# Kernel tuning notes

Measured on AMD Instinct MI355X. Metric: run time of the kernel, lower is better.

## Reference

```python
import jax, jax.numpy as jnp
import numpy as np

NH = 8          # n_heads
EPS = 1e-12     # layer_norm_eps


def _ln(x, g, b, eps=EPS):
    m = x.mean(-1, keepdims=True)
    v = jnp.var(x, axis=-1, keepdims=True)
    return (x - m) / jnp.sqrt(v + eps) * g + b


def _heads(x):
    # [B,S,H] -> [B,NH,S,H/NH]
    B, S, H = x.shape
    return x.reshape(B, S, NH, H // NH).transpose(0, 2, 1, 3)


def setup_inputs() -> dict:
    B, S, H, INNER = 32, 512, 512, 2048
    n_items = 50000
    std = 0.02
    ks = list(jax.random.split(jax.random.key(0), 20))
    inp = {}
    inp['x'] = jax.random.normal(ks[0], (B, S, H), jnp.float32)
    inp['value_input'] = jax.random.normal(ks[1], (B, S, H), jnp.float32)
    inp['beha_emb'] = jax.random.normal(ks[2], (B, S, H), jnp.float32)
    inp['pos_table'] = std * jax.random.normal(ks[3], (S, H), jnp.float32)
    names = ['q', 'k', 'v', 'pk', 'pq', 'bk', 'bq', 'd']
    for i, n in enumerate(names):
        inp['W' + n] = std * jax.random.normal(ks[4 + i], (H, H), jnp.float32)
        inp['b' + n] = jnp.zeros((H,), jnp.float32)
    inp['ln_g'] = jnp.ones((H,), jnp.float32)
    inp['ln_b'] = jnp.zeros((H,), jnp.float32)
    inp['W1'] = std * jax.random.normal(ks[12], (H, INNER), jnp.float32)
    inp['b1'] = jnp.zeros((INNER,), jnp.float32)
    inp['W2'] = std * jax.random.normal(ks[13], (INNER, H), jnp.float32)
    inp['b2'] = jnp.zeros((H,), jnp.float32)
    inp['ln2_g'] = jnp.ones((H,), jnp.float32)
    inp['ln2_b'] = jnp.zeros((H,), jnp.float32)
    inp['item_seq'] = jax.random.randint(ks[14], (B, S), 0, n_items, jnp.int32)
    return inp


def reference(x, value_input, beha_emb, pos_table, Wq, bq, Wk, bk, Wv, bv,
              Wpk, bpk, Wpq, bpq, Wbk, bbk, Wbq, bbq, Wd, bd, ln_g, ln_b,
              W1, b1, W2, b2, ln2_g, ln2_b, item_seq):
    B, S, H = x.shape
    dh = H // NH
    pos = pos_table[:S][None]  # [1,S,H] position_embedding(arange(S))

    q = _heads(x @ Wq + bq)
    k = _heads(x @ Wk + bk)
    v = _heads(value_input @ Wv + bv + value_input)  # value(value_input) + value_input
    pk = _heads(jnp.broadcast_to(pos @ Wpk + bpk, (B, S, H)))
    pq = _heads(jnp.broadcast_to(pos @ Wpq + bpq, (B, S, H)))
    bhk = _heads(beha_emb @ Wbk + bbk)
    bhq = _heads(beha_emb @ Wbq + bbq)

    # disentangled score: q.k^T + q.((beha_k+pos_k)/2)^T + ((beha_q+pos_q)/2).k^T
    scores = (jnp.einsum('bhqd,bhkd->bhqk', q, k)
              + jnp.einsum('bhqd,bhkd->bhqk', q, (bhk + pk) * 0.5)
              + jnp.einsum('bhqd,bhkd->bhqk', (bhq + pq) * 0.5, k))
    scores = scores / (dh ** 0.5)

    # causal + padding mask: (1 - mask) * -10000
    valid = item_seq > 0                              # [B,S]
    causal = jnp.tril(jnp.ones((S, S), bool))         # [S,S]
    ok = valid[:, None, None, :] & causal[None, None]
    scores = scores + jnp.where(ok, 0.0, -10000.0)

    probs = jax.nn.softmax(scores, axis=-1)
    ctx = jnp.einsum('bhqk,bhkd->bhqd', probs, v)
    ctx = ctx.transpose(0, 2, 1, 3).reshape(B, S, H)

    attn_out = _ln(ctx @ Wd + bd + x, ln_g, ln_b)

    # FeedForward (RecBole): dense1 -> gelu -> dense2 -> LN(residual)
    h = jax.nn.gelu(attn_out @ W1 + b1, approximate=False)
    h = h @ W2 + b2
    return _ln(h + attn_out, ln2_g, ln2_b)
```

## Files before the change

kernel.cpp:

```cpp
#include <hip/hip_runtime.h>
#include <math.h>


typedef unsigned short u16;
typedef __attribute__((ext_vector_type(8))) short bf16x8;
typedef __attribute__((ext_vector_type(4))) float f32x4;

#define NM 16384

__device__ __forceinline__ u16 f2b(float f) {
  union { float f; unsigned u; } x; x.f = f;
  return (u16)((x.u + 0x7fffu + ((x.u >> 16) & 1u)) >> 16);
}
__device__ __forceinline__ float b2f(u16 u) {
  union { unsigned u; float f; } x; x.u = ((unsigned)u) << 16; return x.f;
}
__device__ __forceinline__ f32x4 mfma16(bf16x8 a, bf16x8 b, f32x4 c) {
  return __builtin_amdgcn_mfma_f32_16x16x32_bf16(a, b, c, 0, 0, 0);
}
__device__ __forceinline__ void gl16(const u16* g, u16* l) {
  __builtin_amdgcn_global_load_lds(
      (const __attribute__((address_space(1))) unsigned int*)(const void*)g,
      (__attribute__((address_space(3))) unsigned int*)(void*)l, 16, 0, 0);
}

__device__ __forceinline__ void gemm_kloop(
    const u16* pa, const u16* pb, size_t lda, size_t ldb, int kiters,
    const u16* As, const u16* Bs, u16* sa, u16* sb, f32x4 (&acc)[4][4])
{
  const int tid = threadIdx.x;
  const int wave = tid>>6, lane = tid&63, quad = lane>>4, l16 = lane&15;
  const int wm = wave>>1, wn = wave&1;
  const int sw = l16 & 7;
  for (int it = 0; it < kiters; ++it) {
    const u16* pak = pa + it*64;
    const u16* pbk = pb + it*64;
    gl16(pak,          sa);
    gl16(pak + 32*lda, sa + 2048);
    gl16(pak + 64*lda, sa + 4096);
    gl16(pak + 96*lda, sa + 6144);
    gl16(pbk,          sb);
    gl16(pbk + 32*ldb, sb + 2048);
    gl16(pbk + 64*ldb, sb + 4096);
    gl16(pbk + 96*ldb, sb + 6144);
    __syncthreads();
    #pragma unroll
    for (int ks = 0; ks < 2; ++ks) {
      bf16x8 af[4], bf[4];
      #pragma unroll
      for (int i = 0; i < 4; ++i)
        af[i] = *(const bf16x8*)&As[(wm*64 + i*16 + l16)*64 + (((ks*4+quad)^sw)*8)];
      #pragma unroll
      for (int j = 0; j < 4; ++j)
        bf[j] = *(const bf16x8*)&Bs[(wn*64 + j*16 + l16)*64 + (((ks*4+quad)^sw)*8)];
      #pragma unroll
      for (int i = 0; i < 4; ++i)
        #pragma unroll
        for (int j = 0; j < 4; ++j)
          acc[i][j] = mfma16(af[i], bf[j], acc[i][j]);
    }
    __syncthreads();
  }
}

__device__ __forceinline__ const u16* stage_src(const u16* M, int r0, size_t ld) {
  const int tid = threadIdx.x;
  return M + (size_t)(r0 + (tid>>3))*ld + (size_t)(((tid&7) ^ ((tid>>3)&7))*8);
}

__global__ __launch_bounds__(256) void cast_all_kernel(
    const float* __restrict__ x, const float* __restrict__ v,
    const float* __restrict__ be, const float* __restrict__ pos,
    u16* __restrict__ xb, u16* __restrict__ vb, u16* __restrict__ bb,
    u16* __restrict__ posb)
{
  int z = blockIdx.y;
  const float* in = (z==0) ? x : (z==1) ? v : (z==2) ? be : pos;
  u16* out = (z==0) ? xb : (z==1) ? vb : (z==2) ? bb : posb;
  int n4 = (z < 3) ? (NM*512/4) : (512*512/4);
  int i = blockIdx.x*256 + threadIdx.x;
  if (i >= n4) return;
  float4 w = ((const float4*)in)[i];
  ((ushort4*)out)[i] = make_ushort4(f2b(w.x), f2b(w.y), f2b(w.z), f2b(w.w));
}

struct PrepArgs {
  const float* w[10];
  u16* o[10];
  const float* bq; const float* bbq; const float* bbk;
  float* Bq2; float* Bk2;
};
__global__ __launch_bounds__(256) void wprep_all_kernel(PrepArgs a) {
  int job = blockIdx.x;
  if (job == 1024) {
    for (int i = threadIdx.x; i < 512; i += 256) {
      a.Bq2[i] = a.bq[i] + 0.5f*a.bbq[i];
      a.Bk2[i] = 0.5f*a.bbk[i];
    }
    return;
  }
  int wsel, n0, k0, K, N;
  if (job < 512)      { wsel = job>>6; int t = job&63;  n0=(t&7)*64;  k0=(t>>3)*64; K=512;  N=512; }
  else if (job < 768) { wsel = 8;      int t = job-512; n0=(t&31)*64; k0=(t>>5)*64; K=512;  N=2048; }
  else                { wsel = 9;      int t = job-768; n0=(t&7)*64;  k0=(t>>3)*64; K=2048; N=512; }
  float sc = (wsel == 5 || wsel == 6) ? 0.5f : 1.0f;
  const float* in = a.w[wsel];
  u16* out = a.o[wsel];
  __shared__ __align__(16) u16 til[64*72];
  for (int idx = threadIdx.x; idx < 4096; idx += 256) {
    int r = idx>>6, c = idx&63;
    til[r*72+c] = f2b(in[(size_t)(k0+r)*N + n0+c] * sc);
  }
  __syncthreads();
  for (int idx = threadIdx.x; idx < 4096; idx += 256) {
    int r = idx>>6, c = idx&63;
    out[(size_t)(n0+r)*K + k0+c] = til[c*72+r];
  }
}

__global__ __launch_bounds__(256, 3) void gemm_pos_kernel(
    const u16* __restrict__ posb, const u16* __restrict__ WTpq,
    const u16* __restrict__ WTpk, const float* __restrict__ bpq,
    const float* __restrict__ bpk, float* __restrict__ PQh,
    float* __restrict__ PKh)
{
  __shared__ __align__(16) u16 As[128*64];
  __shared__ __align__(16) u16 Bs[128*64];
  const int z = blockIdx.z;
  const u16* W = z ? WTpk : WTpq;
  const float* bias = z ? bpk : bpq;
  float* out = z ? PKh : PQh;
  const int tid = threadIdx.x;
  const int wave = tid>>6, lane = tid&63, quad = lane>>4, l16 = lane&15;
  const int wm = wave>>1, wn = wave&1;
  const int m0 = blockIdx.y*128, n0 = blockIdx.x*128;
  f32x4 acc[4][4] = {};
  gemm_kloop(stage_src(posb + (size_t)m0*512, 0, 512), stage_src(W + (size_t)n0*512, 0, 512),
             512, 512, 8, As, Bs, &As[tid*8], &Bs[tid*8], acc);
  #pragma unroll
  for (int j = 0; j < 4; ++j) {
    int gn = n0 + wn*64 + j*16 + l16;
    float bv = bias[gn];
    #pragma unroll
    for (int i = 0; i < 4; ++i) {
      int gm = m0 + wm*64 + i*16 + quad*4;
      #pragma unroll
      for (int r = 0; r < 4; ++r)
        out[(size_t)(gm+r)*512 + gn] = (acc[i][j][r] + bv)*0.5f;
    }
  }
}

__global__ __launch_bounds__(256, 3) void gemm_qk_kernel(
    const u16* __restrict__ xb, const u16* __restrict__ bb,
    const u16* __restrict__ WTq, const u16* __restrict__ WTk,
    const u16* __restrict__ WTbq, const u16* __restrict__ WTbk,
    const float* __restrict__ bq, const float* __restrict__ bk,
    const float* __restrict__ Bq2, const float* __restrict__ Bk2,
    const float* __restrict__ PQh, const float* __restrict__ PKh,
    u16* __restrict__ Qt, u16* __restrict__ Kt)
{
  __shared__ __align__(16) u16 As[128*64];
  __shared__ __align__(16) u16 Bs[128*64];
  const int z = blockIdx.z;
  const u16* W1 = z ? WTk : WTq;
  const u16* W2 = z ? WTbk : WTbq;
  const float* b1 = z ? bk : bq;
  const float* b2 = z ? Bk2 : Bq2;
  const float* ex = z ? PKh : PQh;
  u16* out = z ? Kt : Qt;
  const float scl = z ? 1.0f : 0.125f;
  const int tid = threadIdx.x;
  const int wave = tid>>6, lane = tid&63, quad = lane>>4, l16 = lane&15;
  const int wm = wave>>1, wn = wave&1;
  const int m0 = blockIdx.y*128, n0 = blockIdx.x*128;
  u16* sa = &As[tid*8];  u16* sb = &Bs[tid*8];

  f32x4 acc[4][4] = {};
  gemm_kloop(stage_src(xb + (size_t)m0*512, 0, 512), stage_src(W1 + (size_t)n0*512, 0, 512),
             512, 512, 8, As, Bs, sa, sb, acc);
  {
    const int hoff = z ? 0 : 64;
    #pragma unroll
    for (int j = 0; j < 4; ++j) {
      int gn = n0 + wn*64 + j*16 + l16;
      float bv = b1[gn];
      size_t col = (size_t)((gn>>6)*128 + (gn&63) + hoff);
      #pragma unroll
      for (int i = 0; i < 4; ++i) {
        int gm = m0 + wm*64 + i*16 + quad*4;
        #pragma unroll
        for (int r = 0; r < 4; ++r)
          out[(size_t)(gm+r)*1024 + col] = f2b((acc[i][j][r] + bv)*scl);
      }
    }
  }
  if (z) {
    #pragma unroll
    for (int i = 0; i < 4; ++i)
      #pragma unroll
      for (int j = 0; j < 4; ++j)
        acc[i][j] = f32x4{0.f, 0.f, 0.f, 0.f};
  }
  gemm_kloop(stage_src(bb + (size_t)m0*512, 0, 512), stage_src(W2 + (size_t)n0*512, 0, 512),
             512, 512, 8, As, Bs, sa, sb, acc);
  {
    const int hoff = z ? 64 : 0;
    #pragma unroll
    for (int j = 0; j < 4; ++j) {
      int gn = n0 + wn*64 + j*16 + l16;
      float bv = b2[gn];
      size_t col = (size_t)((gn>>6)*128 + (gn&63) + hoff);
      #pragma unroll
      for (int i = 0; i < 4; ++i) {
        int gm = m0 + wm*64 + i*16 + quad*4;
        #pragma unroll
        for (int r = 0; r < 4; ++r)
          out[(size_t)(gm+r)*1024 + col] =
              f2b((acc[i][j][r] + bv + ex[(size_t)((gm+r)&511)*512 + gn])*scl);
      }
    }
  }
}

template<int EPI>
__global__ __launch_bounds__(256, 3) void gemm_epi_kernel(
    const u16* __restrict__ A, const u16* __restrict__ W,
    const float* __restrict__ bias, const void* __restrict__ extra,
    void* __restrict__ outp, int M, int N, int K)
{
  __shared__ __align__(16) u16 As[128*64];
  __shared__ __align__(16) u16 Bs[128*64];
  const int tid = threadIdx.x;
  const int wave = tid>>6, lane = tid&63, quad = lane>>4, l16 = lane&15;
  const int wm = wave>>1, wn = wave&1;
  const int m0 = blockIdx.y*128, n0 = blockIdx.x*128;
  f32x4 acc[4][4] = {};
  gemm_kloop(stage_src(A + (size_t)m0*K, 0, K), stage_src(W + (size_t)n0*K, 0, K),
             K, K, K>>6, As, Bs, &As[tid*8], &Bs[tid*8], acc);
  #pragma unroll
  for (int j = 0; j < 4; ++j) {
    int gn = n0 + wn*64 + j*16 + l16;
    float bv = bias[gn];
    #pragma unroll
    for (int i = 0; i < 4; ++i) {
      int gmb = m0 + wm*64 + i*16 + quad*4;
      #pragma unroll
      for (int r = 0; r < 4; ++r) {
        int gm = gmb + r;
        float v = acc[i][j][r] + bv;
        if (EPI == 0) {
          ((float*)outp)[(size_t)gm*N + gn] = v;
        } else if (EPI == 4) {
          v = 0.5f*v*(1.0f + erff(v*0.70710678118654752f));
          ((u16*)outp)[(size_t)gm*N + gn] = f2b(v);
        } else if (EPI == 7) {
          v += b2f(((const u16*)extra)[(size_t)gm*512 + gn]);
          int b = gm>>9, s = gm&511, h = gn>>6, d = gn&63;
          ((u16*)outp)[(size_t)((b*8 + h)*64 + d)*512 + s] = f2b(v);
        } else if (EPI == 8) {
          v += b2f(((const u16*)extra)[(size_t)gm*512 + gn]);
          ((float*)outp)[(size_t)gm*N + gn] = v;
        }
      }
    }
  }
}

__global__ __launch_bounds__(512, 2) void attn_kernel(
    const u16* __restrict__ Qt, const u16* __restrict__ Kt,
    const u16* __restrict__ Vt, const int* __restrict__ iseq,
    u16* __restrict__ ctx)
{
  const int qh = blockIdx.x, h = blockIdx.y, b = blockIdx.z;
  const int tid = threadIdx.x;
  const int wave = tid>>6, lane = tid&63, quad = lane>>4, l16 = lane&15;

  __shared__ __align__(16) u16 Ks[2][64*136];
  __shared__ __align__(16) u16 Vs[2][64*72];
  __shared__ __align__(16) u16 Ps[8][16*72];
  __shared__ float sel[512];

  const int q0 = qh*256;
  const int ntiles = 4*qh + 4;
  const u16* Qg = Qt + (size_t)(b*512)*1024 + h*128;
  const u16* Kg = Kt + (size_t)(b*512)*1024 + h*128;
  const u16* Vg = Vt + (size_t)((b*8 + h)*64)*512;

  if (tid < 512) sel[tid] = (iseq[b*512 + tid] > 0) ? 1.0f : 1e-30f;

  bf16x8 aq[2][4];
  #pragma unroll
  for (int s = 0; s < 2; ++s) {
    const size_t qr = (size_t)(q0 + s*128 + wave*16 + l16)*1024;
    #pragma unroll
    for (int ks = 0; ks < 4; ++ks)
      aq[s][ks] = *(const bf16x8*)&Qg[qr + ks*32 + quad*8];
  }

  const int sr = tid>>3, sc8 = (tid&7)*8, sc16 = (tid&7)*16;
  uint4 kreg0 = *(const uint4*)&Kg[(size_t)sr*1024 + sc16];
  uint4 kreg1 = *(const uint4*)&Kg[(size_t)sr*1024 + sc16 + 8];
  uint4 vreg  = *(const uint4*)&Vg[(size_t)sr*512 + sc8];

  f32x4 Ob[2][4] = {};
  float lrow[2][4] = {};
  u16* Pw = Ps[wave];
  int buf = 0;

  for (int kt = 0; kt < ntiles; ++kt) {
    const int k0 = kt*64;
    *(uint4*)&Ks[buf][sr*136 + sc16]     = kreg0;
    *(uint4*)&Ks[buf][sr*136 + sc16 + 8] = kreg1;
    *(uint4*)&Vs[buf][sr*72 + sc8]       = vreg;
    __syncthreads();
    if (kt + 1 < ntiles) {
      const int kn = k0 + 64;
      kreg0 = *(const uint4*)&Kg[(size_t)(kn + sr)*1024 + sc16];
      kreg1 = *(const uint4*)&Kg[(size_t)(kn + sr)*1024 + sc16 + 8];
      vreg  = *(const uint4*)&Vg[(size_t)sr*512 + kn + sc8];
    }
    const bool act0 = (q0 + wave*16 + 15) >= k0;
    const bool act1 = (q0 + 128 + wave*16 + 15) >= k0;
    if (act1) {
      f32x4 sc[2][4] = {};
      #pragma unroll
      for (int ks = 0; ks < 4; ++ks) {
        bf16x8 bk[4];
        #pragma unroll
        for (int j = 0; j < 4; ++j)
          bk[j] = *(const bf16x8*)&Ks[buf][(j*16 + l16)*136 + ks*32 + quad*8];
        if (act0) {
          #pragma unroll
          for (int j = 0; j < 4; ++j) sc[0][j] = mfma16(aq[0][ks], bk[j], sc[0][j]);
        }
        #pragma unroll
        for (int j = 0; j < 4; ++j) sc[1][j] = mfma16(aq[1][ks], bk[j], sc[1][j]);
      }
      #pragma unroll
      for (int s = 0; s < 2; ++s) {
        if (s == 0 && !act0) continue;
        const int rb = q0 + s*128 + wave*16 + quad*4;
        float pj[4][4];
        #pragma unroll
        for (int j = 0; j < 4; ++j) {
          int col = k0 + j*16 + l16;
          float fs = sel[col];
          #pragma unroll
          for (int r = 0; r < 4; ++r) {
            float m2 = (col <= rb + r) ? fs : 1e-30f;
            pj[j][r] = __expf(sc[s][j][r]) * m2;
          }
        }
        #pragma unroll
        for (int r = 0; r < 4; ++r)
          lrow[s][r] += pj[0][r] + pj[1][r] + pj[2][r] + pj[3][r];
        #pragma unroll
        for (int j = 0; j < 4; ++j)
          #pragma unroll
          for (int r = 0; r < 4; ++r)
            Pw[(quad*4 + r)*72 + j*16 + l16] = f2b(pj[j][r]);
        #pragma unroll
        for (int c = 0; c < 4; ++c) {
          #pragma unroll
          for (int k2 = 0; k2 < 2; ++k2) {
            bf16x8 ap = *(const bf16x8*)&Pw[l16*72 + k2*32 + quad*8];
            bf16x8 bv = *(const bf16x8*)&Vs[buf][(c*16 + l16)*72 + k2*32 + quad*8];
            Ob[s][c] = mfma16(ap, bv, Ob[s][c]);
          }
        }
      }
    }
    buf ^= 1;
  }

  #pragma unroll
  for (int s = 0; s < 2; ++s) {
    #pragma unroll
    for (int r = 0; r < 4; ++r) {
      float l = lrow[s][r];
      #pragma unroll
      for (int d2 = 1; d2 < 16; d2 <<= 1) l += __shfl_xor(l, d2, 64);
      float inv = 1.0f / l;
      int grow = b*512 + q0 + s*128 + wave*16 + quad*4 + r;
      #pragma unroll
      for (int c = 0; c < 4; ++c)
        ctx[(size_t)grow*512 + h*64 + c*16 + l16] = f2b(Ob[s][c][r]*inv);
    }
  }
}

template<int RES>
__global__ __launch_bounds__(256) void ln_kernel(
    const float* __restrict__ a, const void* __restrict__ resv,
    const float* __restrict__ g, const float* __restrict__ be,
    float* __restrict__ of, u16* __restrict__ ob)
{
  const int wave = threadIdx.x >> 6, lane = threadIdx.x & 63;
  const int row = blockIdx.x*4 + wave;
  const float4* pa = (const float4*)(a + (size_t)row*512);
  float4 v0 = pa[lane], v1 = pa[lane+64];
  if (RES == 1) {
    const ushort4* pr = (const ushort4*)((const u16*)resv + (size_t)row*512);
    ushort4 u0 = pr[lane], u1 = pr[lane+64];
    v0.x += b2f(u0.x); v0.y += b2f(u0.y); v0.z += b2f(u0.z); v0.w += b2f(u0.w);
    v1.x += b2f(u1.x); v1.y += b2f(u1.y); v1.z += b2f(u1.z); v1.w += b2f(u1.w);
  } else if (RES == 0) {
    const float4* pr = (const float4*)((const float*)resv + (size_t)row*512);
    float4 r0 = pr[lane], r1 = pr[lane+64];
    v0.x += r0.x; v0.y += r0.y; v0.z += r0.z; v0.w += r0.w;
    v1.x += r1.x; v1.y += r1.y; v1.z += r1.z; v1.w += r1.w;
  }
  float s = v0.x+v0.y+v0.z+v0.w + v1.x+v1.y+v1.z+v1.w;
  float q = v0.x*v0.x+v0.y*v0.y+v0.z*v0.z+v0.w*v0.w
          + v1.x*v1.x+v1.y*v1.y+v1.z*v1.z+v1.w*v1.w;
  #pragma unroll
  for (int d = 1; d < 64; d <<= 1) { s += __shfl_xor(s, d, 64); q += __shfl_xor(q, d, 64); }
  float mean = s * (1.0f/512.0f);
  float var  = q * (1.0f/512.0f) - mean*mean;
  float rstd = rsqrtf(var + 1e-12f);
  float4 g0 = ((const float4*)g)[lane],  g1 = ((const float4*)g)[lane+64];
  float4 b0 = ((const float4*)be)[lane], b1 = ((const float4*)be)[lane+64];
  float4 o0, o1;
  o0.x = (v0.x-mean)*rstd*g0.x + b0.x;  o0.y = (v0.y-mean)*rstd*g0.y + b0.y;
  o0.z = (v0.z-mean)*rstd*g0.z + b0.z;  o0.w = (v0.w-mean)*rstd*g0.w + b0.w;
  o1.x = (v1.x-mean)*rstd*g1.x + b1.x;  o1.y = (v1.y-mean)*rstd*g1.y + b1.y;
  o1.z = (v1.z-mean)*rstd*g1.z + b1.z;  o1.w = (v1.w-mean)*rstd*g1.w + b1.w;
  if (of) {
    ((float4*)(of + (size_t)row*512))[lane]    = o0;
    ((float4*)(of + (size_t)row*512))[lane+64] = o1;
  }
  if (ob) {
    ((ushort4*)(ob + (size_t)row*512))[lane]    = make_ushort4(f2b(o0.x), f2b(o0.y), f2b(o0.z), f2b(o0.w));
    ((ushort4*)(ob + (size_t)row*512))[lane+64] = make_ushort4(f2b(o1.x), f2b(o1.y), f2b(o1.z), f2b(o1.w));
  }
}

extern "C" void kernel_launch(void* const* d_in, const int* in_sizes, int n_in,
                              void* d_out, int out_size, void* d_ws, size_t ws_size,
                              hipStream_t stream) {
  (void)in_sizes; (void)n_in; (void)out_size; (void)ws_size;
  const float* x    = (const float*)d_in[0];
  const float* vin  = (const float*)d_in[1];
  const float* beh  = (const float*)d_in[2];
  const float* pos  = (const float*)d_in[3];
  const float* bq   = (const float*)d_in[5];
  const float* bk   = (const float*)d_in[7];
  const float* bv   = (const float*)d_in[9];
  const float* bpk  = (const float*)d_in[11];
  const float* bpq  = (const float*)d_in[13];
  const float* bbk  = (const float*)d_in[15];
  const float* bbq  = (const float*)d_in[17];
  const float* bd   = (const float*)d_in[19];
  const float* ln_g = (const float*)d_in[20];
  const float* ln_b = (const float*)d_in[21];
  const float* b1   = (const float*)d_in[23];
  const float* b2   = (const float*)d_in[25];
  const float* ln2_g= (const float*)d_in[26];
  const float* ln2_b= (const float*)d_in[27];
  const int*   iseq = (const int*)d_in[28];
  float* out = (float*)d_out;
  char* ws = (char*)d_ws;

  size_t off = 0;
  auto nxt = [&](size_t sz) { size_t r = off; off += (sz + 255) & ~(size_t)255; return r; };
  size_t oWT[8]; for (int i = 0; i < 8; ++i) oWT[i] = nxt(512*512*2);
  size_t oW1T = nxt((size_t)512*2048*2);
  size_t oW2T = nxt((size_t)512*2048*2);
  size_t oBq2 = nxt(512*4);
  size_t oBk2 = nxt(512*4);
  size_t oPb  = nxt(512*512*2);
  size_t oPK  = nxt(512*512*4);
  size_t oPQ  = nxt(512*512*4);
  size_t oXb  = nxt((size_t)NM*512*2);
  size_t oVb  = nxt((size_t)NM*512*2);
  size_t oBb  = nxt((size_t)NM*512*2);
  size_t oR0  = nxt((size_t)NM*512*4);
  size_t oQt  = nxt((size_t)NM*1024*2);
  size_t oKt  = nxt((size_t)NM*1024*2);

  u16* WT[8]; for (int i = 0; i < 8; ++i) WT[i] = (u16*)(ws + oWT[i]);
  u16*   W1T  = (u16*)(ws + oW1T);
  u16*   W2T  = (u16*)(ws + oW2T);
  float* Bq2  = (float*)(ws + oBq2);
  float* Bk2  = (float*)(ws + oBk2);
  u16*   posb = (u16*)(ws + oPb);
  float* PKh  = (float*)(ws + oPK);
  float* PQh  = (float*)(ws + oPQ);
  u16*   xb   = (u16*)(ws + oXb);
  u16*   vb   = (u16*)(ws + oVb);
  u16*   bb   = (u16*)(ws + oBb);
  float* R0   = (float*)(ws + oR0);
  u16*   Qtb  = (u16*)(ws + oQt);
  u16*   Ktb  = (u16*)(ws + oKt);
  u16*   Vtb  = (u16*)(ws + oBb);
  u16*   Cb   = (u16*)(ws + oVb);
  u16*   ab   = (u16*)(ws + oXb);
  u16*   h1b  = (u16*)(ws + oQt);

  cast_all_kernel<<<dim3(8192, 4), 256, 0, stream>>>(x, vin, beh, pos, xb, vb, bb, posb);
  PrepArgs pa;
  const int wi[10] = {4, 6, 8, 10, 12, 14, 16, 18, 22, 24};
  for (int i = 0; i < 10; ++i) pa.w[i] = (const float*)d_in[wi[i]];
  for (int i = 0; i < 8; ++i)  pa.o[i] = WT[i];
  pa.o[8] = W1T; pa.o[9] = W2T;
  pa.bq = bq; pa.bbq = bbq; pa.bbk = bbk; pa.Bq2 = Bq2; pa.Bk2 = Bk2;
  wprep_all_kernel<<<1025, 256, 0, stream>>>(pa);
  gemm_pos_kernel<<<dim3(4, 4, 2), 256, 0, stream>>>(posb, WT[4], WT[3], bpq, bpk, PQh, PKh);
  gemm_qk_kernel<<<dim3(4, 128, 2), 256, 0, stream>>>(
      xb, bb, WT[0], WT[1], WT[6], WT[5], bq, bk, Bq2, Bk2, PQh, PKh, Qtb, Ktb);
  gemm_epi_kernel<7><<<dim3(4, 128), 256, 0, stream>>>(vb, WT[2], bv, vb, Vtb, NM, 512, 512);
  attn_kernel<<<dim3(2, 8, 32), 512, 0, stream>>>(Qtb, Ktb, Vtb, iseq, Cb);
  gemm_epi_kernel<8><<<dim3(4, 128), 256, 0, stream>>>(Cb, WT[7], bd, xb, R0, NM, 512, 512);
  ln_kernel<2><<<4096, 256, 0, stream>>>(R0, nullptr, ln_g, ln_b, nullptr, ab);
  gemm_epi_kernel<4><<<dim3(16, 128), 256, 0, stream>>>(ab, W1T, b1, nullptr, h1b, NM, 2048, 512);
  gemm_epi_kernel<0><<<dim3(4, 128), 256, 0, stream>>>(h1b, W2T, b2, nullptr, R0, NM, 512, 2048);
  ln_kernel<1><<<4096, 256, 0, stream>>>(R0, ab, ln2_g, ln2_b, out, nullptr);
}
```

Baseline: 529.3 us.

## Restructure projections into one batched kernel with bf16 staged epilogues

Replaces the separate pos/qk/value GEMM kernels with a single batched projection kernel covering five projections, using a 32-wide k-step and LDS-staged vectorized bf16 epilogues. Q+P combination now happens in the attention kernel's Q fragment load instead of a fused Qt/Kt layout. Residual outputs (dense, FFN2) are stored as bf16 instead of fp32, and the first LayerNorm reads the fp32 x residual directly. The value residual is added from LDS inside the k-loop. The aim is fewer launches, less memory traffic and coalesced stores, at the cost of less k-work per barrier, lower occupancy (2 blocks per CU), and extra bf16 rounding.

```diff
diff --git a/kernel.cpp b/kernel.cpp
--- a/kernel.cpp
+++ b/kernel.cpp
@@ -23,49 +23,166 @@
       (const __attribute__((address_space(1))) unsigned int*)(const void*)g,
       (__attribute__((address_space(3))) unsigned int*)(void*)l, 16, 0, 0);
 }
-
-__device__ __forceinline__ void gemm_kloop(
-    const u16* pa, const u16* pb, size_t lda, size_t ldb, int kiters,
-    const u16* As, const u16* Bs, u16* sa, u16* sb, f32x4 (&acc)[4][4])
+__device__ __forceinline__ bf16x8 baddv(bf16x8 a, bf16x8 b) {
+  bf16x8 r;
+  #pragma unroll
+  for (int e = 0; e < 8; ++e) r[e] = (short)f2b(b2f((u16)a[e]) + b2f((u16)b[e]));
+  return r;
+}
+
+__device__ __forceinline__ void kloop(
+    const u16* __restrict__ A, const u16* __restrict__ W,
+    int m0, int n0, int K, int kiters, u16* As, u16* Bs, bool vres,
+    f32x4 (&acc)[4][4])
 {
   const int tid = threadIdx.x;
   const int wave = tid>>6, lane = tid&63, quad = lane>>4, l16 = lane&15;
   const int wm = wave>>1, wn = wave&1;
-  const int sw = l16 & 7;
+  const int r1 = tid>>2, ch1 = (tid&3)*8;
+  const u16* pA = A + (size_t)(m0+r1)*K + ch1;
+  const u16* pB = W + (size_t)(n0+r1)*K + ch1;
+  u16* sa = As + tid*8;  u16* sb = Bs + tid*8;
   for (int it = 0; it < kiters; ++it) {
-    const u16* pak = pa + it*64;
-    const u16* pbk = pb + it*64;
-    gl16(pak,          sa);
-    gl16(pak + 32*lda, sa + 2048);
-    gl16(pak + 64*lda, sa + 4096);
-    gl16(pak + 96*lda, sa + 6144);
-    gl16(pbk,          sb);
-    gl16(pbk + 32*ldb, sb + 2048);
-    gl16(pbk + 64*ldb, sb + 4096);
-    gl16(pbk + 96*ldb, sb + 6144);
-    __syncthreads();
+    const int k0 = it*32;
+    gl16(pA + k0, sa); gl16(pA + (size_t)64*K + k0, sa + 2048);
+    gl16(pB + k0, sb); gl16(pB + (size_t)64*K + k0, sb + 2048);
+    __syncthreads();
+    bf16x8 af[4], bf[4];
     #pragma unroll
-    for (int ks = 0; ks < 2; ++ks) {
-      bf16x8 af[4], bf[4];
-      #pragma unroll
-      for (int i = 0; i < 4; ++i)
-        af[i] = *(const bf16x8*)&As[(wm*64 + i*16 + l16)*64 + (((ks*4+quad)^sw)*8)];
+    for (int i = 0; i < 4; ++i)
+      af[i] = *(const bf16x8*)&As[(wm*64 + i*16 + l16)*32 + quad*8];
+    #pragma unroll
+    for (int j = 0; j < 4; ++j)
+      bf[j] = *(const bf16x8*)&Bs[(wn*64 + j*16 + l16)*32 + quad*8];
+    if (vres) {
+      #pragma unroll
+      for (int j = 0; j < 4; ++j) {
+        const int start = n0 + wn*64 + j*16;
+        if ((start & ~31) == k0) {
+          const int c = (start & 31) + l16;
+          #pragma unroll
+          for (int i = 0; i < 4; ++i)
+            #pragma unroll
+            for (int rr = 0; rr < 4; ++rr)
+              acc[i][j][rr] += b2f(As[(wm*64 + i*16 + quad*4 + rr)*32 + c]);
+        }
+      }
+    }
+    #pragma unroll
+    for (int i = 0; i < 4; ++i)
       #pragma unroll
       for (int j = 0; j < 4; ++j)
-        bf[j] = *(const bf16x8*)&Bs[(wn*64 + j*16 + l16)*64 + (((ks*4+quad)^sw)*8)];
-      #pragma unroll
-      for (int i = 0; i < 4; ++i)
-        #pragma unroll
-        for (int j = 0; j < 4; ++j)
-          acc[i][j] = mfma16(af[i], bf[j], acc[i][j]);
-    }
-    __syncthreads();
-  }
-}
-
-__device__ __forceinline__ const u16* stage_src(const u16* M, int r0, size_t ld) {
+        acc[i][j] = mfma16(af[i], bf[j], acc[i][j]);
+    __syncthreads();
+  }
+}
+
+__device__ __forceinline__ void epi_std(
+    f32x4 (&acc)[4][4], const float* __restrict__ bias,
+    const u16* __restrict__ ex, int exmode, float scale, int gelu,
+    u16* __restrict__ out, int m0, int n0, int N, u16* til)
+{
   const int tid = threadIdx.x;
-  return M + (size_t)(r0 + (tid>>3))*ld + (size_t)(((tid&7) ^ ((tid>>3)&7))*8);
+  const int wave = tid>>6, lane = tid&63, quad = lane>>4, l16 = lane&15;
+  const int wm = wave>>1, wn = wave&1;
+  #pragma unroll
+  for (int pass = 0; pass < 2; ++pass) {
+    if (wm == pass) {
+      #pragma unroll
+      for (int j = 0; j < 4; ++j) {
+        const int c = wn*64 + j*16 + l16;
+        const float bv = bias[n0 + c];
+        #pragma unroll
+        for (int i = 0; i < 4; ++i)
+          #pragma unroll
+          for (int rr = 0; rr < 4; ++rr) {
+            float v = acc[i][j][rr] + bv;
+            if (gelu) v = 0.5f*v*(1.0f + erff(v*0.70710678118654752f));
+            til[(i*16 + quad*4 + rr)*136 + c] = f2b(v);
+          }
+      }
+    }
+    __syncthreads();
+    const int r = tid>>2, ck = tid&3;
+    const int gr = m0 + pass*64 + r;
+    #pragma unroll
+    for (int kk = 0; kk < 4; ++kk) {
+      const int cc = ck*32 + kk*8, gc = n0 + cc;
+      u16 e8[8];
+      *(uint4*)e8 = *(const uint4*)&til[r*136 + cc];
+      if (exmode) {
+        const u16* ep = (exmode == 1) ? &ex[(size_t)(gr & 511)*512 + gc]
+                                      : &ex[(size_t)gr*512 + gc];
+        #pragma unroll
+        for (int e = 0; e < 8; ++e) e8[e] = f2b((b2f(e8[e]) + b2f(ep[e]))*scale);
+      } else if (scale != 1.0f) {
+        #pragma unroll
+        for (int e = 0; e < 8; ++e) e8[e] = f2b(b2f(e8[e])*scale);
+      }
+      *(uint4*)&out[(size_t)gr*N + gc] = *(uint4*)e8;
+    }
+    __syncthreads();
+  }
+}
+
+__device__ __forceinline__ void epi_vt(
+    f32x4 (&acc)[4][4], const float* __restrict__ bias,
+    u16* __restrict__ Vt, int m0, int n0, u16* til)
+{
+  const int tid = threadIdx.x;
+  const int wave = tid>>6, lane = tid&63, quad = lane>>4, l16 = lane&15;
+  const int wm = wave>>1, wn = wave&1;
+  const int b = m0 >> 9, s0 = m0 & 511;
+  #pragma unroll
+  for (int pass = 0; pass < 2; ++pass) {
+    if (wn == pass) {
+      #pragma unroll
+      for (int j = 0; j < 4; ++j) {
+        const int cl = j*16 + l16;
+        const float bv = bias[n0 + pass*64 + cl];
+        #pragma unroll
+        for (int i = 0; i < 4; ++i)
+          #pragma unroll
+          for (int rr = 0; rr < 4; ++rr)
+            til[cl*136 + wm*64 + i*16 + quad*4 + rr] = f2b(acc[i][j][rr] + bv);
+      }
+    }
+    __syncthreads();
+    const int cl = tid>>2, ck = tid&3;
+    const int gn = n0 + pass*64 + cl, h = gn>>6, d = gn&63;
+    u16* orow = Vt + ((size_t)((b*8 + h)*64 + d))*512 + s0 + ck*32;
+    #pragma unroll
+    for (int kk = 0; kk < 4; ++kk)
+      *(uint4*)&orow[kk*8] = *(const uint4*)&til[cl*136 + ck*32 + kk*8];
+    __syncthreads();
+  }
+}
+
+struct PJ { const u16* A; const u16* W; const float* bias; const u16* ex;
+            u16* out; float scale; int exmode; int epiv; };
+struct ProjArgs { PJ p[7]; };
+
+__global__ __launch_bounds__(256, 2) void proj_kernel(ProjArgs pa, int phaseBase) {
+  __shared__ __align__(16) u16 smem[8704];
+  u16* As = smem;  u16* Bs = smem + 4096;
+  const PJ P = pa.p[phaseBase + (blockIdx.x >> 2)];
+  const int n0 = (blockIdx.x & 3)*128, m0 = blockIdx.y*128;
+  f32x4 acc[4][4] = {};
+  kloop(P.A, P.W, m0, n0, 512, 16, As, Bs, P.epiv != 0, acc);
+  if (P.epiv) epi_vt(acc, P.bias, P.out, m0, n0, smem);
+  else        epi_std(acc, P.bias, P.ex, P.exmode, P.scale, 0, P.out, m0, n0, 512, smem);
+}
+
+template<int GELU>
+__global__ __launch_bounds__(256, 2) void gemm1_kernel(
+    const u16* __restrict__ A, const u16* __restrict__ W,
+    const float* __restrict__ bias, u16* __restrict__ out, int N, int K)
+{
+  __shared__ __align__(16) u16 smem[8704];
+  const int m0 = blockIdx.y*128, n0 = blockIdx.x*128;
+  f32x4 acc[4][4] = {};
+  kloop(A, W, m0, n0, K, K>>5, smem, smem + 4096, false, acc);
+  epi_std(acc, bias, nullptr, 0, 1.0f, GELU, out, m0, n0, N, smem);
 }
 
 __global__ __launch_bounds__(256) void cast_all_kernel(
@@ -87,14 +204,14 @@
 struct PrepArgs {
   const float* w[10];
   u16* o[10];
-  const float* bq; const float* bbq; const float* bbk;
+  const float* bbq; const float* bbk;
   float* Bq2; float* Bk2;
 };
 __global__ __launch_bounds__(256) void wprep_all_kernel(PrepArgs a) {
   int job = blockIdx.x;
   if (job == 1024) {
     for (int i = threadIdx.x; i < 512; i += 256) {
-      a.Bq2[i] = a.bq[i] + 0.5f*a.bbq[i];
+      a.Bq2[i] = 0.5f*a.bbq[i];
       a.Bk2[i] = 0.5f*a.bbk[i];
     }
     return;
@@ -118,157 +235,9 @@
   }
 }
 
-__global__ __launch_bounds__(256, 3) void gemm_pos_kernel(
-    const u16* __restrict__ posb, const u16* __restrict__ WTpq,
-    const u16* __restrict__ WTpk, const float* __restrict__ bpq,
-    const float* __restrict__ bpk, float* __restrict__ PQh,
-    float* __restrict__ PKh)
-{
-  __shared__ __align__(16) u16 As[128*64];
-  __shared__ __align__(16) u16 Bs[128*64];
-  const int z = blockIdx.z;
-  const u16* W = z ? WTpk : WTpq;
-  const float* bias = z ? bpk : bpq;
-  float* out = z ? PKh : PQh;
-  const int tid = threadIdx.x;
-  const int wave = tid>>6, lane = tid&63, quad = lane>>4, l16 = lane&15;
-  const int wm = wave>>1, wn = wave&1;
-  const int m0 = blockIdx.y*128, n0 = blockIdx.x*128;
-  f32x4 acc[4][4] = {};
-  gemm_kloop(stage_src(posb + (size_t)m0*512, 0, 512), stage_src(W + (size_t)n0*512, 0, 512),
-             512, 512, 8, As, Bs, &As[tid*8], &Bs[tid*8], acc);
-  #pragma unroll
-  for (int j = 0; j < 4; ++j) {
-    int gn = n0 + wn*64 + j*16 + l16;
-    float bv = bias[gn];
-    #pragma unroll
-    for (int i = 0; i < 4; ++i) {
-      int gm = m0 + wm*64 + i*16 + quad*4;
-      #pragma unroll
-      for (int r = 0; r < 4; ++r)
-        out[(size_t)(gm+r)*512 + gn] = (acc[i][j][r] + bv)*0.5f;
-    }
-  }
-}
-
-__global__ __launch_bounds__(256, 3) void gemm_qk_kernel(
-    const u16* __restrict__ xb, const u16* __restrict__ bb,
-    const u16* __restrict__ WTq, const u16* __restrict__ WTk,
-    const u16* __restrict__ WTbq, const u16* __restrict__ WTbk,
-    const float* __restrict__ bq, const float* __restrict__ bk,
-    const float* __restrict__ Bq2, const float* __restrict__ Bk2,
-    const float* __restrict__ PQh, const float* __restrict__ PKh,
-    u16* __restrict__ Qt, u16* __restrict__ Kt)
-{
-  __shared__ __align__(16) u16 As[128*64];
-  __shared__ __align__(16) u16 Bs[128*64];
-  const int z = blockIdx.z;
-  const u16* W1 = z ? WTk : WTq;
-  const u16* W2 = z ? WTbk : WTbq;
-  const float* b1 = z ? bk : bq;
-  const float* b2 = z ? Bk2 : Bq2;
-  const float* ex = z ? PKh : PQh;
-  u16* out = z ? Kt : Qt;
-  const float scl = z ? 1.0f : 0.125f;
-  const int tid = threadIdx.x;
-  const int wave = tid>>6, lane = tid&63, quad = lane>>4, l16 = lane&15;
-  const int wm = wave>>1, wn = wave&1;
-  const int m0 = blockIdx.y*128, n0 = blockIdx.x*128;
-  u16* sa = &As[tid*8];  u16* sb = &Bs[tid*8];
-
-  f32x4 acc[4][4] = {};
-  gemm_kloop(stage_src(xb + (size_t)m0*512, 0, 512), stage_src(W1 + (size_t)n0*512, 0, 512),
-             512, 512, 8, As, Bs, sa, sb, acc);
-  {
-    const int hoff = z ? 0 : 64;
-    #pragma unroll
-    for (int j = 0; j < 4; ++j) {
-      int gn = n0 + wn*64 + j*16 + l16;
-      float bv = b1[gn];
-      size_t col = (size_t)((gn>>6)*128 + (gn&63) + hoff);
-      #pragma unroll
-      for (int i = 0; i < 4; ++i) {
-        int gm = m0 + wm*64 + i*16 + quad*4;
-        #pragma unroll
-        for (int r = 0; r < 4; ++r)
-          out[(size_t)(gm+r)*1024 + col] = f2b((acc[i][j][r] + bv)*scl);
-      }
-    }
-  }
-  if (z) {
-    #pragma unroll
-    for (int i = 0; i < 4; ++i)
-      #pragma unroll
-      for (int j = 0; j < 4; ++j)
-        acc[i][j] = f32x4{0.f, 0.f, 0.f, 0.f};
-  }
-  gemm_kloop(stage_src(bb + (size_t)m0*512, 0, 512), stage_src(W2 + (size_t)n0*512, 0, 512),
-             512, 512, 8, As, Bs, sa, sb, acc);
-  {
-    const int hoff = z ? 64 : 0;
-    #pragma unroll
-    for (int j = 0; j < 4; ++j) {
-      int gn = n0 + wn*64 + j*16 + l16;
-      float bv = b2[gn];
-      size_t col = (size_t)((gn>>6)*128 + (gn&63) + hoff);
-      #pragma unroll
-      for (int i = 0; i < 4; ++i) {
-        int gm = m0 + wm*64 + i*16 + quad*4;
-        #pragma unroll
-        for (int r = 0; r < 4; ++r)
-          out[(size_t)(gm+r)*1024 + col] =
-              f2b((acc[i][j][r] + bv + ex[(size_t)((gm+r)&511)*512 + gn])*scl);
-      }
-    }
-  }
-}
-
-template<int EPI>
-__global__ __launch_bounds__(256, 3) void gemm_epi_kernel(
-    const u16* __restrict__ A, const u16* __restrict__ W,
-    const float* __restrict__ bias, const void* __restrict__ extra,
-    void* __restrict__ outp, int M, int N, int K)
-{
-  __shared__ __align__(16) u16 As[128*64];
-  __shared__ __align__(16) u16 Bs[128*64];
-  const int tid = threadIdx.x;
-  const int wave = tid>>6, lane = tid&63, quad = lane>>4, l16 = lane&15;
-  const int wm = wave>>1, wn = wave&1;
-  const int m0 = blockIdx.y*128, n0 = blockIdx.x*128;
-  f32x4 acc[4][4] = {};
-  gemm_kloop(stage_src(A + (size_t)m0*K, 0, K), stage_src(W + (size_t)n0*K, 0, K),
-             K, K, K>>6, As, Bs, &As[tid*8], &Bs[tid*8], acc);
-  #pragma unroll
-  for (int j = 0; j < 4; ++j) {
-    int gn = n0 + wn*64 + j*16 + l16;
-    float bv = bias[gn];
-    #pragma unroll
-    for (int i = 0; i < 4; ++i) {
-      int gmb = m0 + wm*64 + i*16 + quad*4;
-      #pragma unroll
-      for (int r = 0; r < 4; ++r) {
-        int gm = gmb + r;
-        float v = acc[i][j][r] + bv;
-        if (EPI == 0) {
-          ((float*)outp)[(size_t)gm*N + gn] = v;
-        } else if (EPI == 4) {
-          v = 0.5f*v*(1.0f + erff(v*0.70710678118654752f));
-          ((u16*)outp)[(size_t)gm*N + gn] = f2b(v);
-        } else if (EPI == 7) {
-          v += b2f(((const u16*)extra)[(size_t)gm*512 + gn]);
-          int b = gm>>9, s = gm&511, h = gn>>6, d = gn&63;
-          ((u16*)outp)[(size_t)((b*8 + h)*64 + d)*512 + s] = f2b(v);
-        } else if (EPI == 8) {
-          v += b2f(((const u16*)extra)[(size_t)gm*512 + gn]);
-          ((float*)outp)[(size_t)gm*N + gn] = v;
-        }
-      }
-    }
-  }
-}
-
 __global__ __launch_bounds__(512, 2) void attn_kernel(
-    const u16* __restrict__ Qt, const u16* __restrict__ Kt,
+    const u16* __restrict__ Qraw, const u16* __restrict__ Praw,
+    const u16* __restrict__ Kraw, const u16* __restrict__ Mraw,
     const u16* __restrict__ Vt, const int* __restrict__ iseq,
     u16* __restrict__ ctx)
 {
@@ -283,8 +252,8 @@
 
   const int q0 = qh*256;
   const int ntiles = 4*qh + 4;
-  const u16* Qg = Qt + (size_t)(b*512)*1024 + h*128;
-  const u16* Kg = Kt + (size_t)(b*512)*1024 + h*128;
+  const u16* Kg = Kraw + (size_t)(b*512)*512 + h*64;
+  const u16* Mg = Mraw + (size_t)(b*512)*512 + h*64;
   const u16* Vg = Vt + (size_t)((b*8 + h)*64)*512;
 
   if (tid < 512) sel[tid] = (iseq[b*512 + tid] > 0) ? 1.0f : 1e-30f;
@@ -292,16 +261,19 @@
   bf16x8 aq[2][4];
   #pragma unroll
   for (int s = 0; s < 2; ++s) {
-    const size_t qr = (size_t)(q0 + s*128 + wave*16 + l16)*1024;
-    #pragma unroll
-    for (int ks = 0; ks < 4; ++ks)
-      aq[s][ks] = *(const bf16x8*)&Qg[qr + ks*32 + quad*8];
-  }
-
-  const int sr = tid>>3, sc8 = (tid&7)*8, sc16 = (tid&7)*16;
-  uint4 kreg0 = *(const uint4*)&Kg[(size_t)sr*1024 + sc16];
-  uint4 kreg1 = *(const uint4*)&Kg[(size_t)sr*1024 + sc16 + 8];
-  uint4 vreg  = *(const uint4*)&Vg[(size_t)sr*512 + sc8];
+    const size_t ro = (size_t)(b*512 + q0 + s*128 + wave*16 + l16)*512 + h*64;
+    bf16x8 qf0 = *(const bf16x8*)&Qraw[ro + quad*8];
+    bf16x8 qf1 = *(const bf16x8*)&Qraw[ro + 32 + quad*8];
+    bf16x8 pf0 = *(const bf16x8*)&Praw[ro + quad*8];
+    bf16x8 pf1 = *(const bf16x8*)&Praw[ro + 32 + quad*8];
+    aq[s][0] = baddv(qf0, pf0); aq[s][1] = baddv(qf1, pf1);
+    aq[s][2] = qf0;             aq[s][3] = qf1;
+  }
+
+  const int sr = tid>>3, sc8 = (tid&7)*8;
+  uint4 kreg = *(const uint4*)&Kg[(size_t)sr*512 + sc8];
+  uint4 mreg = *(const uint4*)&Mg[(size_t)sr*512 + sc8];
+  uint4 vreg = *(const uint4*)&Vg[(size_t)sr*512 + sc8];
 
   f32x4 Ob[2][4] = {};
   float lrow[2][4] = {};
@@ -310,15 +282,15 @@
 
   for (int kt = 0; kt < ntiles; ++kt) {
     const int k0 = kt*64;
-    *(uint4*)&Ks[buf][sr*136 + sc16]     = kreg0;
-    *(uint4*)&Ks[buf][sr*136 + sc16 + 8] = kreg1;
+    *(uint4*)&Ks[buf][sr*136 + sc8]      = kreg;
+    *(uint4*)&Ks[buf][sr*136 + 64 + sc8] = mreg;
     *(uint4*)&Vs[buf][sr*72 + sc8]       = vreg;
     __syncthreads();
     if (kt + 1 < ntiles) {
       const int kn = k0 + 64;
-      kreg0 = *(const uint4*)&Kg[(size_t)(kn + sr)*1024 + sc16];
-      kreg1 = *(const uint4*)&Kg[(size_t)(kn + sr)*1024 + sc16 + 8];
-      vreg  = *(const uint4*)&Vg[(size_t)sr*512 + kn + sc8];
+      kreg = *(const uint4*)&Kg[(size_t)(kn + sr)*512 + sc8];
+      mreg = *(const uint4*)&Mg[(size_t)(kn + sr)*512 + sc8];
+      vreg = *(const uint4*)&Vg[(size_t)sr*512 + kn + sc8];
     }
     const bool act0 = (q0 + wave*16 + 15) >= k0;
     const bool act1 = (q0 + 128 + wave*16 + 15) >= k0;
@@ -392,28 +364,30 @@
 
 template<int RES>
 __global__ __launch_bounds__(256) void ln_kernel(
-    const float* __restrict__ a, const void* __restrict__ resv,
+    const u16* __restrict__ a, const void* __restrict__ resv,
     const float* __restrict__ g, const float* __restrict__ be,
     float* __restrict__ of, u16* __restrict__ ob)
 {
   const int wave = threadIdx.x >> 6, lane = threadIdx.x & 63;
   const int row = blockIdx.x*4 + wave;
-  const float4* pa = (const float4*)(a + (size_t)row*512);
-  float4 v0 = pa[lane], v1 = pa[lane+64];
+  const ushort4* pa = (const ushort4*)(a + (size_t)row*512);
+  ushort4 a0 = pa[lane], a1 = pa[lane+64];
+  float v[8] = { b2f(a0.x), b2f(a0.y), b2f(a0.z), b2f(a0.w),
+                 b2f(a1.x), b2f(a1.y), b2f(a1.z), b2f(a1.w) };
   if (RES == 1) {
     const ushort4* pr = (const ushort4*)((const u16*)resv + (size_t)row*512);
     ushort4 u0 = pr[lane], u1 = pr[lane+64];
-    v0.x += b2f(u0.x); v0.y += b2f(u0.y); v0.z += b2f(u0.z); v0.w += b2f(u0.w);
-    v1.x += b2f(u1.x); v1.y += b2f(u1.y); v1.z += b2f(u1.z); v1.w += b2f(u1.w);
-  } else if (RES == 0) {
+    v[0]+=b2f(u0.x); v[1]+=b2f(u0.y); v[2]+=b2f(u0.z); v[3]+=b2f(u0.w);
+    v[4]+=b2f(u1.x); v[5]+=b2f(u1.y); v[6]+=b2f(u1.z); v[7]+=b2f(u1.w);
+  } else {
     const float4* pr = (const float4*)((const float*)resv + (size_t)row*512);
     float4 r0 = pr[lane], r1 = pr[lane+64];
-    v0.x += r0.x; v0.y += r0.y; v0.z += r0.z; v0.w += r0.w;
-    v1.x += r1.x; v1.y += r1.y; v1.z += r1.z; v1.w += r1.w;
-  }
-  float s = v0.x+v0.y+v0.z+v0.w + v1.x+v1.y+v1.z+v1.w;
-  float q = v0.x*v0.x+v0.y*v0.y+v0.z*v0.z+v0.w*v0.w
-          + v1.x*v1.x+v1.y*v1.y+v1.z*v1.z+v1.w*v1.w;
+    v[0]+=r0.x; v[1]+=r0.y; v[2]+=r0.z; v[3]+=r0.w;
+    v[4]+=r1.x; v[5]+=r1.y; v[6]+=r1.z; v[7]+=r1.w;
+  }
+  float s = 0.f, q = 0.f;
+  #pragma unroll
+  for (int e = 0; e < 8; ++e) { s += v[e]; q += v[e]*v[e]; }
   #pragma unroll
   for (int d = 1; d < 64; d <<= 1) { s += __shfl_xor(s, d, 64); q += __shfl_xor(q, d, 64); }
   float mean = s * (1.0f/512.0f);
@@ -421,18 +395,18 @@
   float rstd = rsqrtf(var + 1e-12f);
   float4 g0 = ((const float4*)g)[lane],  g1 = ((const float4*)g)[lane+64];
   float4 b0 = ((const float4*)be)[lane], b1 = ((const float4*)be)[lane+64];
-  float4 o0, o1;
-  o0.x = (v0.x-mean)*rstd*g0.x + b0.x;  o0.y = (v0.y-mean)*rstd*g0.y + b0.y;
-  o0.z = (v0.z-mean)*rstd*g0.z + b0.z;  o0.w = (v0.w-mean)*rstd*g0.w + b0.w;
-  o1.x = (v1.x-mean)*rstd*g1.x + b1.x;  o1.y = (v1.y-mean)*rstd*g1.y + b1.y;
-  o1.z = (v1.z-mean)*rstd*g1.z + b1.z;  o1.w = (v1.w-mean)*rstd*g1.w + b1.w;
+  float o[8];
+  o[0]=(v[0]-mean)*rstd*g0.x+b0.x; o[1]=(v[1]-mean)*rstd*g0.y+b0.y;
+  o[2]=(v[2]-mean)*rstd*g0.z+b0.z; o[3]=(v[3]-mean)*rstd*g0.w+b0.w;
+  o[4]=(v[4]-mean)*rstd*g1.x+b1.x; o[5]=(v[5]-mean)*rstd*g1.y+b1.y;
+  o[6]=(v[6]-mean)*rstd*g1.z+b1.z; o[7]=(v[7]-mean)*rstd*g1.w+b1.w;
   if (of) {
-    ((float4*)(of + (size_t)row*512))[lane]    = o0;
-    ((float4*)(of + (size_t)row*512))[lane+64] = o1;
+    ((float4*)(of + (size_t)row*512))[lane]    = make_float4(o[0],o[1],o[2],o[3]);
+    ((float4*)(of + (size_t)row*512))[lane+64] = make_float4(o[4],o[5],o[6],o[7]);
   }
   if (ob) {
-    ((ushort4*)(ob + (size_t)row*512))[lane]    = make_ushort4(f2b(o0.x), f2b(o0.y), f2b(o0.z), f2b(o0.w));
-    ((ushort4*)(ob + (size_t)row*512))[lane+64] = make_ushort4(f2b(o1.x), f2b(o1.y), f2b(o1.z), f2b(o1.w));
+    ((ushort4*)(ob + (size_t)row*512))[lane]    = make_ushort4(f2b(o[0]),f2b(o[1]),f2b(o[2]),f2b(o[3]));
+    ((ushort4*)(ob + (size_t)row*512))[lane+64] = make_ushort4(f2b(o[4]),f2b(o[5]),f2b(o[6]),f2b(o[7]));
   }
 }
 
@@ -470,14 +444,16 @@
   size_t oBq2 = nxt(512*4);
   size_t oBk2 = nxt(512*4);
   size_t oPb  = nxt(512*512*2);
-  size_t oPK  = nxt(512*512*4);
-  size_t oPQ  = nxt(512*512*4);
+  size_t oPQ  = nxt(512*512*2);
+  size_t oPK  = nxt(512*512*2);
   size_t oXb  = nxt((size_t)NM*512*2);
   size_t oVb  = nxt((size_t)NM*512*2);
   size_t oBb  = nxt((size_t)NM*512*2);
-  size_t oR0  = nxt((size_t)NM*512*4);
-  size_t oQt  = nxt((size_t)NM*1024*2);
-  size_t oKt  = nxt((size_t)NM*1024*2);
+  size_t oQr  = nxt((size_t)NM*512*2);
+  size_t oPr  = nxt((size_t)NM*512*2);
+  size_t oKr  = nxt((size_t)NM*512*2);
+  size_t oMr  = nxt((size_t)NM*512*2);
+  size_t oVt  = nxt((size_t)NM*512*2);
 
   u16* WT[8]; for (int i = 0; i < 8; ++i) WT[i] = (u16*)(ws + oWT[i]);
   u16*   W1T  = (u16*)(ws + oW1T);
@@ -485,35 +461,44 @@
   float* Bq2  = (float*)(ws + oBq2);
   float* Bk2  = (float*)(ws + oBk2);
   u16*   posb = (u16*)(ws + oPb);
-  float* PKh  = (float*)(ws + oPK);
-  float* PQh  = (float*)(ws + oPQ);
+  u16*   PQs  = (u16*)(ws + oPQ);
+  u16*   PKs  = (u16*)(ws + oPK);
   u16*   xb   = (u16*)(ws + oXb);
   u16*   vb   = (u16*)(ws + oVb);
   u16*   bb   = (u16*)(ws + oBb);
-  float* R0   = (float*)(ws + oR0);
-  u16*   Qtb  = (u16*)(ws + oQt);
-  u16*   Ktb  = (u16*)(ws + oKt);
-  u16*   Vtb  = (u16*)(ws + oBb);
+  u16*   Qraw = (u16*)(ws + oQr);
+  u16*   Praw = (u16*)(ws + oPr);
+  u16*   Kraw = (u16*)(ws + oKr);
+  u16*   Mraw = (u16*)(ws + oMr);
+  u16*   Vtb  = (u16*)(ws + oVt);
   u16*   Cb   = (u16*)(ws + oVb);
+  u16*   db   = (u16*)(ws + oPr);
   u16*   ab   = (u16*)(ws + oXb);
-  u16*   h1b  = (u16*)(ws + oQt);
+  u16*   h1b  = (u16*)(ws + oQr);
+  u16*   f2   = (u16*)(ws + oVt);
 
   cast_all_kernel<<<dim3(8192, 4), 256, 0, stream>>>(x, vin, beh, pos, xb, vb, bb, posb);
-  PrepArgs pa;
+  PrepArgs pr;
   const int wi[10] = {4, 6, 8, 10, 12, 14, 16, 18, 22, 24};
-  for (int i = 0; i < 10; ++i) pa.w[i] = (const float*)d_in[wi[i]];
-  for (int i = 0; i < 8; ++i)  pa.o[i] = WT[i];
-  pa.o[8] = W1T; pa.o[9] = W2T;
-  pa.bq = bq; pa.bbq = bbq; pa.bbk = bbk; pa.Bq2 = Bq2; pa.Bk2 = Bk2;
-  wprep_all_kernel<<<1025, 256, 0, stream>>>(pa);
-  gemm_pos_kernel<<<dim3(4, 4, 2), 256, 0, stream>>>(posb, WT[4], WT[3], bpq, bpk, PQh, PKh);
-  gemm_qk_kernel<<<dim3(4, 128, 2), 256, 0, stream>>>(
-      xb, bb, WT[0], WT[1], WT[6], WT[5], bq, bk, Bq2, Bk2, PQh, PKh, Qtb, Ktb);
-  gemm_epi_kernel<7><<<dim3(4, 128), 256, 0, stream>>>(vb, WT[2], bv, vb, Vtb, NM, 512, 512);
-  attn_kernel<<<dim3(2, 8, 32), 512, 0, stream>>>(Qtb, Ktb, Vtb, iseq, Cb);
-  gemm_epi_kernel<8><<<dim3(4, 128), 256, 0, stream>>>(Cb, WT[7], bd, xb, R0, NM, 512, 512);
-  ln_kernel<2><<<4096, 256, 0, stream>>>(R0, nullptr, ln_g, ln_b, nullptr, ab);
-  gemm_epi_kernel<4><<<dim3(16, 128), 256, 0, stream>>>(ab, W1T, b1, nullptr, h1b, NM, 2048, 512);
-  gemm_epi_kernel<0><<<dim3(4, 128), 256, 0, stream>>>(h1b, W2T, b2, nullptr, R0, NM, 512, 2048);
-  ln_kernel<1><<<4096, 256, 0, stream>>>(R0, ab, ln2_g, ln2_b, out, nullptr);
-}
+  for (int i = 0; i < 10; ++i) pr.w[i] = (const float*)d_in[wi[i]];
+  for (int i = 0; i < 8; ++i)  pr.o[i] = WT[i];
+  pr.o[8] = W1T; pr.o[9] = W2T;
+  pr.bbq = bbq; pr.bbk = bbk; pr.Bq2 = Bq2; pr.Bk2 = Bk2;
+  wprep_all_kernel<<<1025, 256, 0, stream>>>(pr);
+  ProjArgs pj;
+  pj.p[0] = { xb,   WT[0], bq,   nullptr, Qraw, 0.125f, 0, 0 };
+  pj.p[1] = { xb,   WT[1], bk,   nullptr, Kraw, 1.0f,   0, 0 };
+  pj.p[2] = { bb,   WT[6], Bq2,  PQs,     Praw, 0.125f, 1, 0 };
+  pj.p[3] = { bb,   WT[5], Bk2,  PKs,     Mraw, 1.0f,   1, 0 };
+  pj.p[4] = { vb,   WT[2], bv,   nullptr, Vtb,  1.0f,   0, 1 };
+  pj.p[5] = { posb, WT[4], bpq,  nullptr, PQs,  0.5f,   0, 0 };
+  pj.p[6] = { posb, WT[3], bpk,  nullptr, PKs,  0.5f,   0, 0 };
+  proj_kernel<<<dim3(8, 4), 256, 0, stream>>>(pj, 5);
+  proj_kernel<<<dim3(20, 128), 256, 0, stream>>>(pj, 0);
+  attn_kernel<<<dim3(2, 8, 32), 512, 0, stream>>>(Qraw, Praw, Kraw, Mraw, Vtb, iseq, Cb);
+  gemm1_kernel<0><<<dim3(4, 128), 256, 0, stream>>>(Cb, WT[7], bd, db, 512, 512);
+  ln_kernel<0><<<4096, 256, 0, stream>>>(db, x, ln_g, ln_b, nullptr, ab);
+  gemm1_kernel<1><<<dim3(16, 128), 256, 0, stream>>>(ab, W1T, b1, h1b, 2048, 512);
+  gemm1_kernel<0><<<dim3(4, 128), 256, 0, stream>>>(h1b, W2T, b2, f2, 512, 2048);
+  ln_kernel<1><<<4096, 256, 0, stream>>>(f2, ab, ln2_g, ln2_b, out, nullptr);
+}
```

New measurement: 515.8 us. 2.5% less time.
